# Kernel optimization log

Hardware: AMD Instinct MI355X
Metric: run time of the kernel (lower is better)

The kernel has to match this reference:

```python
import jax, jax.numpy as jnp
from jax import lax
import numpy as np

VOCAB, L, D, K = 50000, 8921, 300, 10
B, T = 8, 2048


def setup_inputs() -> dict:
    key = jax.random.key(0)
    k_ids, k_e, k_cw, k_cb, k_u = jax.random.split(key, 5)
    ids = jax.random.randint(k_ids, (B, T), 0, VOCAB, dtype=jnp.int32)
    embed_w = jax.random.normal(k_e, (VOCAB, D), dtype=jnp.float32) * 0.02
    embed_w = embed_w.at[0].set(0.0)  # padding_idx=0
    conv_w = jax.random.normal(k_cw, (D, D, K), dtype=jnp.float32) * 0.02  # (out, in, k) == torch OIH
    conv_b = jax.random.normal(k_cb, (D,), dtype=jnp.float32) * 0.02
    U = jax.random.normal(k_u, (L, D), dtype=jnp.float32)
    fc_bias = jnp.zeros((L,), dtype=jnp.float32)
    return {"ids": ids, "embed_w": embed_w, "conv_w": conv_w, "conv_b": conv_b, "U": U, "fc_bias": fc_bias}


def reference(ids, embed_w, conv_w, conv_b, U, fc_bias):
    # Embedding lookup (padding_idx row already zeroed in table)
    e = embed_w[ids]                       # (B, T, D)
    x = jnp.transpose(e, (0, 2, 1))        # (B, D, T)
    pad = conv_w.shape[-1] - 1             # torch padding=filter_size-1 (both sides)
    h = lax.conv_general_dilated(
        x, conv_w, window_strides=(1,), padding=[(pad, pad)],
        dimension_numbers=("NCH", "OIH", "NCH"))
    h = jax.nn.relu(h + conv_b[None, :, None])   # (B, D, T') where T' = T + K - 1
    attn = jax.nn.softmax(jnp.einsum("ld,bdt->blt", U, h), axis=-1)  # (B, L, T')
    z = jnp.einsum("blt,bdt->bld", attn, h)                          # (B, L, D)
    logits = jnp.einsum("bld,ld->bl", z, U) + fc_bias                # (B, L)
    return logits
```

## Files before the change

kernel.cpp:

```cpp
#include <hip/hip_runtime.h>

#define VOCAB   50000
#define LDIM    8921
#define DDIM    300
#define DPAD    320
#define KSZ     10
#define BATCH   8
#define TSEQ    2048
#define PADL    9
#define TPRIME  2057
#define TPADDED 2066
#define LPAD    8928

#define TSTG    32
#define NTT     65
#define TALLOC  (NTT * TSTG)
#define LBLK    70

typedef short s8v __attribute__((ext_vector_type(8)));
typedef float f4v __attribute__((ext_vector_type(4)));

typedef const __attribute__((address_space(1))) unsigned int* gas_ptr;
typedef __attribute__((address_space(3))) unsigned int* las_ptr;

__device__ inline unsigned short f2bf(float f) {
  union { float f; unsigned u; } v; v.f = f;
  unsigned r = v.u + 0x7FFF + ((v.u >> 16) & 1);
  return (unsigned short)(r >> 16);
}

__global__ __launch_bounds__(256) void gather_kernel(
    const int* __restrict__ ids, const float* __restrict__ embed_w,
    unsigned short* __restrict__ xp) {
  int wid = blockIdx.x * 4 + (threadIdx.x >> 6);
  int lane = threadIdx.x & 63;
  int b = wid / TPADDED, tau = wid % TPADDED;
  bool inr = (tau >= PADL) && (tau < PADL + TSEQ);
  int row = inr ? ids[b * TSEQ + (tau - PADL)] : 0;
  const float* src = embed_w + (size_t)row * DDIM;
  unsigned short* dst = xp + ((size_t)b * TPADDED + tau) * DPAD;
  for (int j = 0; j < 5; ++j) {
    int col = j * 64 + lane;
    float v = (inr && col < DDIM) ? src[col] : 0.0f;
    dst[col] = f2bf(v);
  }
}

__global__ __launch_bounds__(256) void wt_kernel(
    const float* __restrict__ w, unsigned short* __restrict__ wT) {
  int k = blockIdx.x / DPAD, o = blockIdx.x % DPAD;
  for (int i = threadIdx.x; i < DPAD; i += 256) {
    float v = (o < DDIM && i < DDIM) ? w[((size_t)o * DDIM + i) * KSZ + k] : 0.0f;
    wT[((size_t)k * DPAD + o) * DPAD + i] = f2bf(v);
  }
}

__global__ __launch_bounds__(256) void ut_kernel(
    const float* __restrict__ U, unsigned short* __restrict__ Ub) {
  int l = blockIdx.x;
  for (int d = threadIdx.x; d < DPAD; d += 256) {
    float v = (l < LDIM && d < DDIM) ? U[(size_t)l * DDIM + d] : 0.0f;
    Ub[(size_t)l * DPAD + d] = f2bf(v);
  }
}

#define CTN 64
#define CROWS 73
#define CSTRIDE 328
__global__ __launch_bounds__(256, 2) void conv_mfma_kernel(
    const unsigned short* __restrict__ xp, const unsigned short* __restrict__ wT,
    const float* __restrict__ bias, unsigned short* __restrict__ h) {
  __shared__ unsigned short xls[CROWS * CSTRIDE];
  int b = blockIdx.x & 7, tb = blockIdx.x >> 3;
  int t0 = tb * CTN;
  int tid = threadIdx.x;
  {
    const unsigned short* src = xp + (size_t)b * TPADDED * DPAD;
    for (int idx = tid; idx < CROWS * (DPAD / 8); idx += 256) {
      int r = idx / 40, c8 = idx % 40;
      int tp = t0 + r;
      int4 v = make_int4(0, 0, 0, 0);
      if (tp < TPADDED) v = *(const int4*)&src[(size_t)tp * DPAD + c8 * 8];
      *(int4*)&xls[r * CSTRIDE + c8 * 8] = v;
    }
  }
  __syncthreads();
  int w = tid >> 6, lane = tid & 63;
  int l15 = lane & 15, quad = lane >> 4;
  f4v acc[5][4];
#pragma unroll
  for (int mf = 0; mf < 5; ++mf) {
    float bv[4];
#pragma unroll
    for (int r = 0; r < 4; ++r) {
      int o = w * 80 + mf * 16 + quad * 4 + r;
      bv[r] = (o < DDIM) ? bias[o] : 0.0f;
    }
#pragma unroll
    for (int nf = 0; nf < 4; ++nf) {
      acc[mf][nf][0] = bv[0]; acc[mf][nf][1] = bv[1];
      acc[mf][nf][2] = bv[2]; acc[mf][nf][3] = bv[3];
    }
  }
  s8v Acur[5], Anext[5];
#pragma unroll
  for (int mf = 0; mf < 5; ++mf)
    Acur[mf] = *(const s8v*)&wT[(size_t)(w * 80 + mf * 16 + l15) * DPAD + quad * 8];
  for (int iter = 0; iter < 100; ++iter) {
    int kc = iter / 10, it = iter % 10;
    if (iter < 99) {
      int kn = (iter + 1) / 10, itn = (iter + 1) % 10;
#pragma unroll
      for (int mf = 0; mf < 5; ++mf)
        Anext[mf] = *(const s8v*)&wT[((size_t)kn * DPAD + w * 80 + mf * 16 + l15) * DPAD + itn * 32 + quad * 8];
    }
    s8v Bv[4];
#pragma unroll
    for (int nf = 0; nf < 4; ++nf) {
      int rrow = nf * 16 + l15 + kc;
      Bv[nf] = *(const s8v*)&xls[rrow * CSTRIDE + it * 32 + quad * 8];
    }
#pragma unroll
    for (int mf = 0; mf < 5; ++mf)
#pragma unroll
      for (int nf = 0; nf < 4; ++nf)
        acc[mf][nf] = __builtin_amdgcn_mfma_f32_16x16x32_bf16(Acur[mf], Bv[nf], acc[mf][nf], 0, 0, 0);
#pragma unroll
    for (int mf = 0; mf < 5; ++mf) Acur[mf] = Anext[mf];
  }
#pragma unroll
  for (int mf = 0; mf < 5; ++mf) {
    int obase = w * 80 + mf * 16 + quad * 4;
#pragma unroll
    for (int nf = 0; nf < 4; ++nf) {
      int t = t0 + nf * 16 + l15;
      if (t < TALLOC) {
        bool live = t < TPRIME;
        unsigned short pk[4];
#pragma unroll
        for (int r = 0; r < 4; ++r)
          pk[r] = live ? f2bf(fmaxf(acc[mf][nf][r], 0.0f)) : (unsigned short)0;
        *(uint2*)&h[((size_t)b * TALLOC + t) * DPAD + obase] = *(uint2*)pk;
      }
    }
  }
}

__global__ __launch_bounds__(256, 3) void attn_mfma_kernel(
    const unsigned short* __restrict__ h, const unsigned short* __restrict__ Ub,
    const float* __restrict__ fcb, float* __restrict__ out) {
  __shared__ unsigned short hls[2 * TSTG * DPAD];
  int b = blockIdx.x & 7, lb = blockIdx.x >> 3;
  int tid = threadIdx.x;
  int w = tid >> 6, lane = tid & 63;
  int l15 = lane & 15, quad = lane >> 4;
  const unsigned short* hb = h + (size_t)b * TALLOC * DPAD;

  s8v A[2][10];
  {
    int lr0 = lb * 128 + w * 32 + l15;
#pragma unroll
    for (int mf = 0; mf < 2; ++mf) {
      int lr = lr0 + mf * 16;
      if (lr >= LPAD) lr = LPAD - 1;
      const unsigned short* up = Ub + (size_t)lr * DPAD + quad * 8;
#pragma unroll
      for (int kc = 0; kc < 10; ++kc)
        A[mf][kc] = *(const s8v*)&up[kc * 32];
    }
  }

  int srcoff[5];
#pragma unroll
  for (int j = 0; j < 5; ++j) {
    int g = w * 320 + j * 64 + lane;
    int r = g / 40, c = g % 40;
    srcoff[j] = r * DPAD + ((c ^ (r & 7)) * 8);
  }

#pragma unroll
  for (int j = 0; j < 5; ++j)
    __builtin_amdgcn_global_load_lds((gas_ptr)(const void*)(hb + srcoff[j]),
                                     (las_ptr)(void*)&hls[w * 2560 + j * 512],
                                     16, 0, 0);
  asm volatile("s_waitcnt vmcnt(0)" ::: "memory");
  __builtin_amdgcn_s_barrier();

  float se[2][4], sw[2][4];
#pragma unroll
  for (int mf = 0; mf < 2; ++mf)
#pragma unroll
    for (int r = 0; r < 4; ++r) { se[mf][r] = 0.0f; sw[mf][r] = 0.0f; }

  int xr8 = (l15 & 7) * 8;
  int rowb0 = l15 * DPAD;
  int rowb1 = (16 + l15) * DPAD;
  int bufsel = 0;
  for (int t = 0; t < NTT; ++t) {
    if (t + 1 < NTT) {
      const unsigned short* src = hb + (size_t)(t + 1) * TSTG * DPAD;
      int dstb = (bufsel ^ 1) * 10240 + w * 2560;
#pragma unroll
      for (int j = 0; j < 5; ++j)
        __builtin_amdgcn_global_load_lds((gas_ptr)(const void*)(src + srcoff[j]),
                                         (las_ptr)(void*)&hls[dstb + j * 512],
                                         16, 0, 0);
    }
    const unsigned short* bufc = &hls[bufsel * 10240];
    f4v acc[2][2];
#pragma unroll
    for (int mf = 0; mf < 2; ++mf)
#pragma unroll
      for (int nf = 0; nf < 2; ++nf) {
        acc[mf][nf][0] = 0.0f; acc[mf][nf][1] = 0.0f;
        acc[mf][nf][2] = 0.0f; acc[mf][nf][3] = 0.0f;
      }
#pragma unroll
    for (int kc = 0; kc < 10; ++kc) {
      int ko = (kc * 32 + quad * 8) ^ xr8;
      s8v Bv0 = *(const s8v*)&bufc[rowb0 + ko];
      s8v Bv1 = *(const s8v*)&bufc[rowb1 + ko];
      acc[0][0] = __builtin_amdgcn_mfma_f32_16x16x32_bf16(A[0][kc], Bv0, acc[0][0], 0, 0, 0);
      acc[0][1] = __builtin_amdgcn_mfma_f32_16x16x32_bf16(A[0][kc], Bv1, acc[0][1], 0, 0, 0);
      acc[1][0] = __builtin_amdgcn_mfma_f32_16x16x32_bf16(A[1][kc], Bv0, acc[1][0], 0, 0, 0);
      acc[1][1] = __builtin_amdgcn_mfma_f32_16x16x32_bf16(A[1][kc], Bv1, acc[1][1], 0, 0, 0);
    }
    int tb0 = t * TSTG;
#pragma unroll
    for (int nf = 0; nf < 2; ++nf) {
      bool valid = (tb0 + nf * 16 + l15) < TPRIME;
#pragma unroll
      for (int mf = 0; mf < 2; ++mf)
#pragma unroll
        for (int r = 0; r < 4; ++r) {
          float s = acc[mf][nf][r];
          float e = valid ? __expf(s) : 0.0f;
          se[mf][r] += e;
          sw[mf][r] = fmaf(e, valid ? s : 0.0f, sw[mf][r]);
        }
    }
    asm volatile("s_waitcnt vmcnt(0)" ::: "memory");
    __builtin_amdgcn_s_barrier();
    bufsel ^= 1;
  }

#pragma unroll
  for (int mf = 0; mf < 2; ++mf)
#pragma unroll
    for (int r = 0; r < 4; ++r) {
      float a = se[mf][r], c = sw[mf][r];
#pragma unroll
      for (int off = 1; off < 16; off <<= 1) {
        a += __shfl_xor(a, off, 64);
        c += __shfl_xor(c, off, 64);
      }
      if (l15 == 0) {
        int l = lb * 128 + w * 32 + mf * 16 + quad * 4 + r;
        if (l < LDIM) out[(size_t)b * LDIM + l] = c / a + fcb[l];
      }
    }
}

extern "C" void kernel_launch(void* const* d_in, const int* in_sizes, int n_in,
                              void* d_out, int out_size, void* d_ws, size_t ws_size,
                              hipStream_t stream) {
  const int*   ids     = (const int*)d_in[0];
  const float* embed_w = (const float*)d_in[1];
  const float* conv_w  = (const float*)d_in[2];
  const float* conv_b  = (const float*)d_in[3];
  const float* U       = (const float*)d_in[4];
  const float* fc_bias = (const float*)d_in[5];
  float* out = (float*)d_out;

  unsigned char* p = (unsigned char*)d_ws;
  unsigned short* xp = (unsigned short*)p;                 p += (size_t)BATCH * TPADDED * DPAD * 2;
  unsigned short* hb = (unsigned short*)p;                 p += (size_t)BATCH * TALLOC * DPAD * 2;
  unsigned short* wT = (unsigned short*)p;                 p += (size_t)KSZ * DPAD * DPAD * 2;
  unsigned short* Ub = (unsigned short*)p;

  hipLaunchKernelGGL(gather_kernel, dim3(BATCH * TPADDED / 4), dim3(256), 0, stream,
                     ids, embed_w, xp);
  hipLaunchKernelGGL(wt_kernel, dim3(KSZ * DPAD), dim3(256), 0, stream, conv_w, wT);
  hipLaunchKernelGGL(ut_kernel, dim3(LPAD), dim3(256), 0, stream, U, Ub);
  hipLaunchKernelGGL(conv_mfma_kernel, dim3(BATCH * 33), dim3(256), 0, stream,
                     xp, wT, conv_b, hb);
  hipLaunchKernelGGL(attn_mfma_kernel, dim3(BATCH * LBLK), dim3(256), 0, stream,
                     hb, Ub, fc_bias, out);
}
```

Before: 336.3 us.

## Shrink conv time tile and split waves over time to raise conv parallelism

The conv kernel now covers 32 time steps per block with 512 threads, where 4 waves split output channels and 2 split time. Each wave holds one time fragment instead of four, and the grid grows from 264 to 520 blocks so the GPU's compute units are better filled. The trade-off is less reuse of each weight fragment: every wave still streams the full 10x320x80 weight slice, so global/L2 weight traffic per time step roughly doubles. The gather kernel also writes packed pairs of bf16 values with 32-bit stores instead of single 16-bit stores.

```diff
diff --git a/kernel.cpp b/kernel.cpp
--- a/kernel.cpp
+++ b/kernel.cpp
@@ -39,10 +39,15 @@
   int row = inr ? ids[b * TSEQ + (tau - PADL)] : 0;
   const float* src = embed_w + (size_t)row * DDIM;
   unsigned short* dst = xp + ((size_t)b * TPADDED + tau) * DPAD;
-  for (int j = 0; j < 5; ++j) {
-    int col = j * 64 + lane;
-    float v = (inr && col < DDIM) ? src[col] : 0.0f;
-    dst[col] = f2bf(v);
+#pragma unroll
+  for (int j = 0; j < 3; ++j) {
+    int c2 = (j * 64 + lane) * 2;
+    if (c2 < DPAD) {
+      float v0 = (inr && c2 < DDIM) ? src[c2] : 0.0f;
+      float v1 = (inr && c2 + 1 < DDIM) ? src[c2 + 1] : 0.0f;
+      unsigned pk = (unsigned)f2bf(v0) | ((unsigned)f2bf(v1) << 16);
+      *(unsigned*)&dst[c2] = pk;
+    }
   }
 }
 
@@ -64,10 +69,10 @@
   }
 }
 
-#define CTN 64
-#define CROWS 73
+#define CTN 32
+#define CROWS 41
 #define CSTRIDE 328
-__global__ __launch_bounds__(256, 2) void conv_mfma_kernel(
+__global__ __launch_bounds__(512, 4) void conv_mfma_kernel(
     const unsigned short* __restrict__ xp, const unsigned short* __restrict__ wT,
     const float* __restrict__ bias, unsigned short* __restrict__ h) {
   __shared__ unsigned short xls[CROWS * CSTRIDE];
@@ -76,7 +81,7 @@
   int tid = threadIdx.x;
   {
     const unsigned short* src = xp + (size_t)b * TPADDED * DPAD;
-    for (int idx = tid; idx < CROWS * (DPAD / 8); idx += 256) {
+    for (int idx = tid; idx < CROWS * (DPAD / 8); idx += 512) {
       int r = idx / 40, c8 = idx % 40;
       int tp = t0 + r;
       int4 v = make_int4(0, 0, 0, 0);
@@ -85,63 +90,50 @@
     }
   }
   __syncthreads();
-  int w = tid >> 6, lane = tid & 63;
+  int ww = tid >> 6, lane = tid & 63;
+  int wo = ww & 3;
+  int wt = ww >> 2;
   int l15 = lane & 15, quad = lane >> 4;
-  f4v acc[5][4];
+  f4v acc[5];
 #pragma unroll
   for (int mf = 0; mf < 5; ++mf) {
-    float bv[4];
 #pragma unroll
     for (int r = 0; r < 4; ++r) {
-      int o = w * 80 + mf * 16 + quad * 4 + r;
-      bv[r] = (o < DDIM) ? bias[o] : 0.0f;
-    }
-#pragma unroll
-    for (int nf = 0; nf < 4; ++nf) {
-      acc[mf][nf][0] = bv[0]; acc[mf][nf][1] = bv[1];
-      acc[mf][nf][2] = bv[2]; acc[mf][nf][3] = bv[3];
+      int o = wo * 80 + mf * 16 + quad * 4 + r;
+      acc[mf][r] = (o < DDIM) ? bias[o] : 0.0f;
     }
   }
   s8v Acur[5], Anext[5];
 #pragma unroll
   for (int mf = 0; mf < 5; ++mf)
-    Acur[mf] = *(const s8v*)&wT[(size_t)(w * 80 + mf * 16 + l15) * DPAD + quad * 8];
+    Acur[mf] = *(const s8v*)&wT[(size_t)(wo * 80 + mf * 16 + l15) * DPAD + quad * 8];
   for (int iter = 0; iter < 100; ++iter) {
     int kc = iter / 10, it = iter % 10;
     if (iter < 99) {
       int kn = (iter + 1) / 10, itn = (iter + 1) % 10;
 #pragma unroll
       for (int mf = 0; mf < 5; ++mf)
-        Anext[mf] = *(const s8v*)&wT[((size_t)kn * DPAD + w * 80 + mf * 16 + l15) * DPAD + itn * 32 + quad * 8];
-    }
-    s8v Bv[4];
-#pragma unroll
-    for (int nf = 0; nf < 4; ++nf) {
-      int rrow = nf * 16 + l15 + kc;
-      Bv[nf] = *(const s8v*)&xls[rrow * CSTRIDE + it * 32 + quad * 8];
-    }
+        Anext[mf] = *(const s8v*)&wT[((size_t)kn * DPAD + wo * 80 + mf * 16 + l15) * DPAD + itn * 32 + quad * 8];
+    }
+    int rrow = wt * 16 + l15 + kc;
+    s8v Bv = *(const s8v*)&xls[rrow * CSTRIDE + it * 32 + quad * 8];
 #pragma unroll
     for (int mf = 0; mf < 5; ++mf)
-#pragma unroll
-      for (int nf = 0; nf < 4; ++nf)
-        acc[mf][nf] = __builtin_amdgcn_mfma_f32_16x16x32_bf16(Acur[mf], Bv[nf], acc[mf][nf], 0, 0, 0);
+      acc[mf] = __builtin_amdgcn_mfma_f32_16x16x32_bf16(Acur[mf], Bv, acc[mf], 0, 0, 0);
 #pragma unroll
     for (int mf = 0; mf < 5; ++mf) Acur[mf] = Anext[mf];
   }
-#pragma unroll
-  for (int mf = 0; mf < 5; ++mf) {
-    int obase = w * 80 + mf * 16 + quad * 4;
-#pragma unroll
-    for (int nf = 0; nf < 4; ++nf) {
-      int t = t0 + nf * 16 + l15;
-      if (t < TALLOC) {
-        bool live = t < TPRIME;
-        unsigned short pk[4];
-#pragma unroll
-        for (int r = 0; r < 4; ++r)
-          pk[r] = live ? f2bf(fmaxf(acc[mf][nf][r], 0.0f)) : (unsigned short)0;
-        *(uint2*)&h[((size_t)b * TALLOC + t) * DPAD + obase] = *(uint2*)pk;
-      }
+  int t = t0 + wt * 16 + l15;
+  if (t < TALLOC) {
+    bool live = t < TPRIME;
+#pragma unroll
+    for (int mf = 0; mf < 5; ++mf) {
+      int obase = wo * 80 + mf * 16 + quad * 4;
+      unsigned short pk[4];
+#pragma unroll
+      for (int r = 0; r < 4; ++r)
+        pk[r] = live ? f2bf(fmaxf(acc[mf][r], 0.0f)) : (unsigned short)0;
+      *(uint2*)&h[((size_t)b * TALLOC + t) * DPAD + obase] = *(uint2*)pk;
     }
   }
 }
@@ -282,7 +274,7 @@
                      ids, embed_w, xp);
   hipLaunchKernelGGL(wt_kernel, dim3(KSZ * DPAD), dim3(256), 0, stream, conv_w, wT);
   hipLaunchKernelGGL(ut_kernel, dim3(LPAD), dim3(256), 0, stream, U, Ub);
-  hipLaunchKernelGGL(conv_mfma_kernel, dim3(BATCH * 33), dim3(256), 0, stream,
+  hipLaunchKernelGGL(conv_mfma_kernel, dim3(BATCH * NTT), dim3(512), 0, stream,
                      xp, wT, conv_b, hb);
   hipLaunchKernelGGL(attn_mfma_kernel, dim3(BATCH * LBLK), dim3(256), 0, stream,
                      hb, Ub, fc_bias, out);
```

Measured after the change: 548.1 us. 63.0% more time.

## Split conv output channels across two blocks and vectorize gather stores

Applied to the files above, without the earlier changes.

The conv kernel now launches twice as many blocks. Each block covers half the output channels (160), and its four waves are arranged as 2 output-channel groups by 2 time groups, so each wave holds a 5x2 accumulator tile instead of 5x4. The goal is to fill more CUs on the 256-CU MI355X, since the old grid had only 264 blocks, and to lower register pressure. The cost is that each block loads the same x tile into LDS, doubling LDS staging traffic. The gather kernel now packs two bf16 values per 32-bit store instead of writing single shorts.

```diff
diff --git a/kernel.cpp b/kernel.cpp
--- a/kernel.cpp
+++ b/kernel.cpp
@@ -39,10 +39,15 @@
   int row = inr ? ids[b * TSEQ + (tau - PADL)] : 0;
   const float* src = embed_w + (size_t)row * DDIM;
   unsigned short* dst = xp + ((size_t)b * TPADDED + tau) * DPAD;
-  for (int j = 0; j < 5; ++j) {
-    int col = j * 64 + lane;
-    float v = (inr && col < DDIM) ? src[col] : 0.0f;
-    dst[col] = f2bf(v);
+#pragma unroll
+  for (int j = 0; j < 3; ++j) {
+    int c2 = (j * 64 + lane) * 2;
+    if (c2 < DPAD) {
+      float v0 = (inr && c2 < DDIM) ? src[c2] : 0.0f;
+      float v1 = (inr && c2 + 1 < DDIM) ? src[c2 + 1] : 0.0f;
+      unsigned pk = (unsigned)f2bf(v0) | ((unsigned)f2bf(v1) << 16);
+      *(unsigned*)&dst[c2] = pk;
+    }
   }
 }
 
@@ -71,33 +76,36 @@
     const unsigned short* __restrict__ xp, const unsigned short* __restrict__ wT,
     const float* __restrict__ bias, unsigned short* __restrict__ h) {
   __shared__ unsigned short xls[CROWS * CSTRIDE];
-  int b = blockIdx.x & 7, tb = blockIdx.x >> 3;
+  int b = blockIdx.x & 7, r = blockIdx.x >> 3;
+  int tb = r >> 1, oh = r & 1;
   int t0 = tb * CTN;
   int tid = threadIdx.x;
   {
     const unsigned short* src = xp + (size_t)b * TPADDED * DPAD;
     for (int idx = tid; idx < CROWS * (DPAD / 8); idx += 256) {
-      int r = idx / 40, c8 = idx % 40;
-      int tp = t0 + r;
+      int rr = idx / 40, c8 = idx % 40;
+      int tp = t0 + rr;
       int4 v = make_int4(0, 0, 0, 0);
       if (tp < TPADDED) v = *(const int4*)&src[(size_t)tp * DPAD + c8 * 8];
-      *(int4*)&xls[r * CSTRIDE + c8 * 8] = v;
+      *(int4*)&xls[rr * CSTRIDE + c8 * 8] = v;
     }
   }
   __syncthreads();
-  int w = tid >> 6, lane = tid & 63;
+  int ww = tid >> 6, lane = tid & 63;
+  int wo = ww & 1, wt = ww >> 1;
   int l15 = lane & 15, quad = lane >> 4;
-  f4v acc[5][4];
+  int ob = oh * 160 + wo * 80;
+  f4v acc[5][2];
 #pragma unroll
   for (int mf = 0; mf < 5; ++mf) {
     float bv[4];
 #pragma unroll
-    for (int r = 0; r < 4; ++r) {
-      int o = w * 80 + mf * 16 + quad * 4 + r;
-      bv[r] = (o < DDIM) ? bias[o] : 0.0f;
-    }
-#pragma unroll
-    for (int nf = 0; nf < 4; ++nf) {
+    for (int rr = 0; rr < 4; ++rr) {
+      int o = ob + mf * 16 + quad * 4 + rr;
+      bv[rr] = (o < DDIM) ? bias[o] : 0.0f;
+    }
+#pragma unroll
+    for (int nf = 0; nf < 2; ++nf) {
       acc[mf][nf][0] = bv[0]; acc[mf][nf][1] = bv[1];
       acc[mf][nf][2] = bv[2]; acc[mf][nf][3] = bv[3];
     }
@@ -105,41 +113,42 @@
   s8v Acur[5], Anext[5];
 #pragma unroll
   for (int mf = 0; mf < 5; ++mf)
-    Acur[mf] = *(const s8v*)&wT[(size_t)(w * 80 + mf * 16 + l15) * DPAD + quad * 8];
+    Acur[mf] = *(const s8v*)&wT[(size_t)(ob + mf * 16 + l15) * DPAD + quad * 8];
+#pragma unroll 10
   for (int iter = 0; iter < 100; ++iter) {
     int kc = iter / 10, it = iter % 10;
     if (iter < 99) {
       int kn = (iter + 1) / 10, itn = (iter + 1) % 10;
 #pragma unroll
       for (int mf = 0; mf < 5; ++mf)
-        Anext[mf] = *(const s8v*)&wT[((size_t)kn * DPAD + w * 80 + mf * 16 + l15) * DPAD + itn * 32 + quad * 8];
-    }
-    s8v Bv[4];
-#pragma unroll
-    for (int nf = 0; nf < 4; ++nf) {
-      int rrow = nf * 16 + l15 + kc;
+        Anext[mf] = *(const s8v*)&wT[((size_t)kn * DPAD + ob + mf * 16 + l15) * DPAD + itn * 32 + quad * 8];
+    }
+    s8v Bv[2];
+#pragma unroll
+    for (int nf = 0; nf < 2; ++nf) {
+      int rrow = wt * 32 + nf * 16 + l15 + kc;
       Bv[nf] = *(const s8v*)&xls[rrow * CSTRIDE + it * 32 + quad * 8];
     }
 #pragma unroll
     for (int mf = 0; mf < 5; ++mf)
 #pragma unroll
-      for (int nf = 0; nf < 4; ++nf)
+      for (int nf = 0; nf < 2; ++nf)
         acc[mf][nf] = __builtin_amdgcn_mfma_f32_16x16x32_bf16(Acur[mf], Bv[nf], acc[mf][nf], 0, 0, 0);
 #pragma unroll
     for (int mf = 0; mf < 5; ++mf) Acur[mf] = Anext[mf];
   }
 #pragma unroll
   for (int mf = 0; mf < 5; ++mf) {
-    int obase = w * 80 + mf * 16 + quad * 4;
-#pragma unroll
-    for (int nf = 0; nf < 4; ++nf) {
-      int t = t0 + nf * 16 + l15;
+    int obase = ob + mf * 16 + quad * 4;
+#pragma unroll
+    for (int nf = 0; nf < 2; ++nf) {
+      int t = t0 + wt * 32 + nf * 16 + l15;
       if (t < TALLOC) {
         bool live = t < TPRIME;
         unsigned short pk[4];
 #pragma unroll
-        for (int r = 0; r < 4; ++r)
-          pk[r] = live ? f2bf(fmaxf(acc[mf][nf][r], 0.0f)) : (unsigned short)0;
+        for (int rr = 0; rr < 4; ++rr)
+          pk[rr] = live ? f2bf(fmaxf(acc[mf][nf][rr], 0.0f)) : (unsigned short)0;
         *(uint2*)&h[((size_t)b * TALLOC + t) * DPAD + obase] = *(uint2*)pk;
       }
     }
@@ -282,7 +291,7 @@
                      ids, embed_w, xp);
   hipLaunchKernelGGL(wt_kernel, dim3(KSZ * DPAD), dim3(256), 0, stream, conv_w, wT);
   hipLaunchKernelGGL(ut_kernel, dim3(LPAD), dim3(256), 0, stream, U, Ub);
-  hipLaunchKernelGGL(conv_mfma_kernel, dim3(BATCH * 33), dim3(256), 0, stream,
+  hipLaunchKernelGGL(conv_mfma_kernel, dim3(BATCH * 33 * 2), dim3(256), 0, stream,
                      xp, wT, conv_b, hb);
   hipLaunchKernelGGL(attn_mfma_kernel, dim3(BATCH * LBLK), dim3(256), 0, stream,
                      hb, Ub, fc_bias, out);
```

New measurement: 390.1 us. 16.0% more time.
